# Performance work log

Measured on AMD Instinct MI355X. Metric: run time of the kernel, lower is better.

Reference implementation:

```python
import jax, jax.numpy as jnp
import numpy as np

V, E, H = 50000, 300, 512
L, N, K = 6, 8192, 4


def setup_inputs() -> dict:
    key = jax.random.key(0)
    ks = jax.random.split(key, 12)
    vocab_ix = jax.random.randint(ks[0], (L, N), 0, V)
    child_idx = jax.random.randint(ks[1], (L, N, K), 0, N)
    token_mask = jnp.ones((L, N), dtype=jnp.float32)
    child_mask = (jax.random.uniform(ks[2], (L, N, K)) < 0.75).astype(jnp.float32)
    s = 0.02
    embed = jax.random.normal(ks[3], (V, E), dtype=jnp.float32)
    W_iou = jax.random.normal(ks[4], (E, 3 * H), dtype=jnp.float32) * s
    U_iou = jax.random.normal(ks[5], (H, 3 * H), dtype=jnp.float32) * s
    b_iou = jnp.zeros((3 * H,), dtype=jnp.float32)
    W_f = jax.random.normal(ks[6], (E, H), dtype=jnp.float32) * s
    U_f = jax.random.normal(ks[7], (H, H), dtype=jnp.float32) * s
    b_f = jnp.zeros((H,), dtype=jnp.float32)
    return {"vocab_ix": vocab_ix, "child_idx": child_idx, "token_mask": token_mask,
            "child_mask": child_mask, "embed": embed, "W_iou": W_iou, "U_iou": U_iou,
            "b_iou": b_iou, "W_f": W_f, "U_f": U_f, "b_f": b_f}


def _tree_lstm(vocab_ix, child_idx, token_mask, child_mask,
               embed, W_iou, U_iou, b_iou, W_f, U_f, b_f):
    # bottom-up over levels; level L-1 = leaves (no children -> zero prev states)
    h = jnp.zeros((N, H), dtype=embed.dtype)
    c = jnp.zeros((N, H), dtype=embed.dtype)
    for l in reversed(range(L)):
        # word2vec: embedding lookup; zero vector for non-token nodes
        x = embed[vocab_ix[l]] * token_mask[l][:, None]            # [N, E]
        xWf = x @ W_f                                              # [N, H]
        if l == L - 1:
            h_tilde = jnp.zeros((N, H), dtype=x.dtype)
            fc = jnp.zeros((N, H), dtype=x.dtype)
        else:
            m = child_mask[l][:, :, None]                          # [N, K, 1]
            h_ch = h[child_idx[l]] * m                             # [N, K, H]
            c_ch = c[child_idx[l]] * m                             # [N, K, H]
            h_tilde = h_ch.sum(axis=1)                             # child-sum
            # per-child forget gates (padded slots: c_ch is 0 -> no contribution)
            f = jax.nn.sigmoid(xWf[:, None, :] + jnp.einsum('nkh,hj->nkj', h_ch, U_f) + b_f)
            fc = (f * c_ch).sum(axis=1)
        iou = x @ W_iou + h_tilde @ U_iou + b_iou                  # [N, 3H]
        i, o, u = jnp.split(iou, 3, axis=-1)
        c = jax.nn.sigmoid(i) * jnp.tanh(u) + fc
        h = jax.nn.sigmoid(o) * jnp.tanh(c)
    return h  # outputs[0][1]: hidden states of root level


def reference(vocab_ix, child_idx, token_mask, child_mask,
              embed, W_iou, U_iou, b_iou, W_f, U_f, b_f):
    return _tree_lstm(vocab_ix, child_idx, token_mask, child_mask,
                      embed, W_iou, U_iou, b_iou, W_f, U_f, b_f)
```

## Files before the change

### kernel.cpp

```cpp
#include <hip/hip_runtime.h>
#include <cmath>

#define VSZ  50000
#define EDIM 300
#define EPAD 320
#define HDIM 512
#define LVLS 6
#define NN   8192
#define KCH  4

#define BM 128
#define BN 128
#define BK 32

typedef __attribute__((ext_vector_type(8))) short bf16x8;
typedef __attribute__((ext_vector_type(8))) unsigned short us8;
typedef __attribute__((ext_vector_type(4))) float f32x4;

__device__ __forceinline__ float sigf(float x) { return 1.0f / (1.0f + expf(-x)); }

__device__ __forceinline__ unsigned short f2bf(float f) {
    unsigned u = __float_as_uint(f);
    u += 0x7FFF + ((u >> 16) & 1);
    return (unsigned short)(u >> 16);
}
__device__ __forceinline__ float bf2f(unsigned short h) {
    return __uint_as_float(((unsigned)h) << 16);
}

__device__ __forceinline__ unsigned cvt_pk_bf16(float lo, float hi) {
    unsigned r;
    asm("v_cvt_pk_bf16_f32 %0, %1, %2" : "=v"(r) : "v"(lo), "v"(hi));
    return r;
}

__global__ __launch_bounds__(256) void gconv_k(
    const float* __restrict__ embed, const int* __restrict__ vix,
    const float* __restrict__ tmask, unsigned short* __restrict__ out)
{
    int t  = blockIdx.x * 256 + threadIdx.x;
    int r  = t / (EPAD / 8);
    int j8 = (t - r * (EPAD / 8)) * 8;
    float m = tmask[r];
    int   v = vix[r];
    const float* src = embed + (size_t)v * EDIM + j8;
    us8 o;
    if (j8 + 8 <= EDIM) {
        float4 a = *(const float4*)(src);
        float4 b = *(const float4*)(src + 4);
        const float xs[8] = {a.x, a.y, a.z, a.w, b.x, b.y, b.z, b.w};
#pragma unroll
        for (int j = 0; j < 8; ++j) o[j] = f2bf(xs[j] * m);
    } else {
#pragma unroll
        for (int j = 0; j < 8; ++j) {
            float x = (j8 + j < EDIM) ? src[j] * m : 0.0f;
            o[j] = f2bf(x);
        }
    }
    *(us8*)(out + (size_t)r * EPAD + j8) = o;
}

__global__ __launch_bounds__(256) void wconv_k(
    const float* __restrict__ in, unsigned short* __restrict__ out,
    int Kreal, int Ksp, int Nd)
{
    int t = blockIdx.x * 256 + threadIdx.x;
    int k = t % Ksp;
    int n = t / Ksp;
    out[t] = (k < Kreal) ? f2bf(in[(size_t)k * Nd + n]) : (unsigned short)0;
}

#define GLL(src, dst)                                                        \
    __builtin_amdgcn_global_load_lds(                                        \
        (const __attribute__((address_space(1))) unsigned int*)(src), (dst), 16, 0, 0)

template <int EPI, int NCHUNK>
__global__ __launch_bounds__(256) void mgemm_k(
    const unsigned short* __restrict__ Ab,
    const unsigned short* __restrict__ Bt,
    const float* __restrict__ b_iou, const float* __restrict__ b_f,
    unsigned short* __restrict__ C, int ldc, int Ks)
{
    __shared__ __align__(16) unsigned short smem[6 * BM * BK];

    const int tid  = threadIdx.x;
    const int wave = tid >> 6;
    const int lane = tid & 63;
    const int quad = lane >> 4;
    const int mcol = lane & 15;
    const int wm   = (wave >> 1) * 64;
    const int wn   = (wave & 1) * 64;
    const int band = wave >> 1;

    const int GX   = gridDim.x;
    const int P    = blockIdx.x + GX * blockIdx.y;
    const int g    = P & 7;
    const int s    = P >> 3;
    const int mper = gridDim.y >> 3;
    const int sdiv = s / GX;
    const int my_mt = g * mper + sdiv;
    const int my_ng = s - sdiv * GX;
    const int tile_m = my_mt * BM;

    const int r0  = tid >> 2;
    const int kg0 = (tid & 3) ^ ((r0 >> 1) & 3);
    const int cc1 = tid + 256;
    const int r1  = cc1 >> 2;
    const int kg1 = (cc1 & 3) ^ ((r1 >> 1) & 3);

    const unsigned short* asrc0 = Ab + (size_t)(tile_m + r0) * Ks + kg0 * 8;
    const unsigned short* asrc1 = Ab + (size_t)(tile_m + r1) * Ks + kg1 * 8;

    typedef __attribute__((address_space(3))) unsigned int lds_u32;

    float* eb = reinterpret_cast<float*>(smem);
    const int erl = tid >> 3;
    const int ecg = tid & 7;

#define STAGE3(kk, bo)                                                       \
    {                                                                        \
        GLL(asrc0 + (kk), (lds_u32*)(smem + (bo) + wave * 512));             \
        GLL(asrc1 + (kk), (lds_u32*)(smem + (bo) + 2048 + wave * 512));      \
        GLL(bsrc0 + (kk), (lds_u32*)(smem + (bo) + 4096 + wave * 512));      \
        GLL(bsrc1 + (kk), (lds_u32*)(smem + (bo) + 6144 + wave * 512));      \
    }
#define WAITV4  asm volatile("s_waitcnt vmcnt(4)" ::: "memory")
#define WAITV0  asm volatile("s_waitcnt vmcnt(0)" ::: "memory")
#define BAR     __builtin_amdgcn_s_barrier()

#define COMPUTE(bo)                                                         \
    {                                                                       \
        const unsigned short* AS = smem + (bo);                             \
        const unsigned short* BS = smem + (bo) + 4096;                      \
        bf16x8 afr[4], bfr[4];                                              \
        _Pragma("unroll")                                                   \
        for (int mt = 0; mt < 4; ++mt) {                                    \
            int rw = wm + mt * 16 + mcol;                                   \
            int p  = rw * 4 + (quad ^ ((rw >> 1) & 3));                     \
            afr[mt] = *(const bf16x8*)(AS + p * 8);                         \
        }                                                                   \
        _Pragma("unroll")                                                   \
        for (int nt = 0; nt < 4; ++nt) {                                    \
            int rw = wn + nt * 16 + mcol;                                   \
            int p  = rw * 4 + (quad ^ ((rw >> 1) & 3));                     \
            bfr[nt] = *(const bf16x8*)(BS + p * 8);                         \
        }                                                                   \
        _Pragma("unroll")                                                   \
        for (int mt = 0; mt < 4; ++mt)                                      \
            _Pragma("unroll")                                               \
            for (int nt = 0; nt < 4; ++nt)                                  \
                acc[mt][nt] = __builtin_amdgcn_mfma_f32_16x16x32_bf16(      \
                    afr[mt], bfr[nt], acc[mt][nt], 0, 0, 0);                \
    }

    for (int nc = 0; nc < NCHUNK; ++nc) {
        const int tile_n = (my_ng * NCHUNK + nc) * BN;
        const unsigned short* bsrc0 = Bt + (size_t)(tile_n + r0) * Ks + kg0 * 8;
        const unsigned short* bsrc1 = Bt + (size_t)(tile_n + r1) * Ks + kg1 * 8;

        f32x4 acc[4][4] = {};
        const int nsteps = Ks / BK;

        int bo0 = 0, bo1 = 8192, bo2 = 16384;

        STAGE3(0, bo0);
        STAGE3(BK, bo1);
        WAITV4;
        BAR;

        for (int st = 0; st < nsteps; ++st) {
            const bool pf = (st + 2 < nsteps);
            if (pf) STAGE3((st + 2) * BK, bo2);
            COMPUTE(bo0);
            if (pf) { WAITV4; } else { WAITV0; }
            BAR;
            int t0 = bo0; bo0 = bo1; bo1 = bo2; bo2 = t0;
        }

#pragma unroll
        for (int mt = 0; mt < 4; ++mt) {
            const int rbase = band * 16 + quad * 4;
#pragma unroll
            for (int nt = 0; nt < 4; ++nt) {
                const int cb = wn + nt * 16 + mcol;
                const int gq = cb >> 2;
                const int cl = cb & 3;
#pragma unroll
                for (int rr = 0; rr < 4; ++rr) {
                    const int r = rbase + rr;
                    eb[r * 128 + ((gq ^ (r & 7)) << 2) + cl] = acc[mt][nt][rr];
                }
            }
            __syncthreads();

            const int grow = tile_m + (erl >> 4) * 64 + mt * 16 + (erl & 15);
            const int gcol = tile_n + ecg * 16;
            float v[16];
#pragma unroll
            for (int sxt = 0; sxt < 4; ++sxt) {
                const int pg = (ecg * 4 + sxt) ^ (erl & 7);
                f32x4 q = *(const f32x4*)&eb[erl * 128 + pg * 4];
                v[sxt * 4 + 0] = q[0]; v[sxt * 4 + 1] = q[1];
                v[sxt * 4 + 2] = q[2]; v[sxt * 4 + 3] = q[3];
            }
            if (EPI == 1) {
                const float* bp = (gcol < 3 * HDIM) ? (b_iou + gcol)
                                                    : (b_f + gcol - 3 * HDIM);
                float4 b0 = *(const float4*)(bp);
                float4 b1 = *(const float4*)(bp + 4);
                float4 b2 = *(const float4*)(bp + 8);
                float4 b3 = *(const float4*)(bp + 12);
                const float bb[16] = {b0.x, b0.y, b0.z, b0.w, b1.x, b1.y, b1.z, b1.w,
                                      b2.x, b2.y, b2.z, b2.w, b3.x, b3.y, b3.z, b3.w};
#pragma unroll
                for (int j = 0; j < 16; ++j) v[j] += bb[j];
            }
            unsigned pw[8];
#pragma unroll
            for (int j = 0; j < 8; ++j) pw[j] = cvt_pk_bf16(v[2 * j], v[2 * j + 1]);
            unsigned short* cp = C + (size_t)grow * ldc + gcol;
            *(uint4*)(cp)     = make_uint4(pw[0], pw[1], pw[2], pw[3]);
            *(uint4*)(cp + 8) = make_uint4(pw[4], pw[5], pw[6], pw[7]);
            __syncthreads();
        }
    }
#undef STAGE3
#undef WAITV4
#undef WAITV0
#undef BAR
#undef COMPUTE
}

template <bool LAST>
__global__ __launch_bounds__(256) void gatefc_k(
    const unsigned short* __restrict__ iouxW, const unsigned short* __restrict__ Z,
    const int* __restrict__ cidx, const float* __restrict__ cmask,
    const float* __restrict__ c_prev,
    float* __restrict__ c_new, unsigned short* __restrict__ hb_new,
    float* __restrict__ h_out)
{
    int t  = blockIdx.x * 256 + threadIdx.x;
    int n  = t >> 6;
    int j8 = (t & 63) << 3;
    const unsigned short* xr = iouxW + (size_t)n * 4 * HDIM + j8;
    us8 xi = *(const us8*)xr;
    us8 xo = *(const us8*)(xr + HDIM);
    us8 xu = *(const us8*)(xr + 2 * HDIM);
    us8 xf = *(const us8*)(xr + 3 * HDIM);
    float ia[8], oa[8], ua[8], xw[8], fc[8];
#pragma unroll
    for (int j = 0; j < 8; ++j) {
        ia[j] = bf2f(xi[j]); oa[j] = bf2f(xo[j]);
        ua[j] = bf2f(xu[j]); xw[j] = bf2f(xf[j]);
        fc[j] = 0.0f;
    }
    int4   ci = *(const int4*)&cidx[n * KCH];
    float4 cm = *(const float4*)&cmask[n * KCH];
    const int   cia[4] = {ci.x, ci.y, ci.z, ci.w};
    const float cma[4] = {cm.x, cm.y, cm.z, cm.w};
#pragma unroll
    for (int k = 0; k < KCH; ++k) {
        const float m = cma[k];
        const unsigned short* zr = Z + (size_t)cia[k] * 4 * HDIM + j8;
        us8 zi = *(const us8*)zr;
        us8 zo = *(const us8*)(zr + HDIM);
        us8 zu = *(const us8*)(zr + 2 * HDIM);
        us8 zf = *(const us8*)(zr + 3 * HDIM);
        const float* cpr = c_prev + (size_t)cia[k] * HDIM + j8;
        float4 ca = *(const float4*)cpr;
        float4 cb = *(const float4*)(cpr + 4);
        const float cp[8] = {ca.x, ca.y, ca.z, ca.w, cb.x, cb.y, cb.z, cb.w};
#pragma unroll
        for (int j = 0; j < 8; ++j) {
            ia[j] += m * bf2f(zi[j]);
            oa[j] += m * bf2f(zo[j]);
            ua[j] += m * bf2f(zu[j]);
            fc[j] += sigf(xw[j] + m * bf2f(zf[j])) * m * cp[j];
        }
    }
    float cv[8], hv[8];
#pragma unroll
    for (int j = 0; j < 8; ++j) {
        cv[j] = sigf(ia[j]) * tanhf(ua[j]) + fc[j];
        hv[j] = sigf(oa[j]) * tanhf(cv[j]);
    }
    if (LAST) {
        float4 h0 = make_float4(hv[0], hv[1], hv[2], hv[3]);
        float4 h1 = make_float4(hv[4], hv[5], hv[6], hv[7]);
        *(float4*)(h_out + (size_t)n * HDIM + j8)     = h0;
        *(float4*)(h_out + (size_t)n * HDIM + j8 + 4) = h1;
    } else {
        float4 c0v = make_float4(cv[0], cv[1], cv[2], cv[3]);
        float4 c1v = make_float4(cv[4], cv[5], cv[6], cv[7]);
        *(float4*)(c_new + (size_t)n * HDIM + j8)     = c0v;
        *(float4*)(c_new + (size_t)n * HDIM + j8 + 4) = c1v;
        us8 hb;
#pragma unroll
        for (int j = 0; j < 8; ++j) hb[j] = f2bf(hv[j]);
        *(us8*)(hb_new + (size_t)n * HDIM + j8) = hb;
    }
}

__global__ __launch_bounds__(256) void gateleaf_k(
    const unsigned short* __restrict__ iouxW,
    float* __restrict__ c_new, unsigned short* __restrict__ hb_new)
{
    int t  = blockIdx.x * 256 + threadIdx.x;
    int n  = t >> 6;
    int j8 = (t & 63) << 3;
    const unsigned short* xr = iouxW + (size_t)n * 4 * HDIM + j8;
    us8 xi = *(const us8*)xr;
    us8 xo = *(const us8*)(xr + HDIM);
    us8 xu = *(const us8*)(xr + 2 * HDIM);
    float cv[8], hv[8];
#pragma unroll
    for (int j = 0; j < 8; ++j) {
        cv[j] = sigf(bf2f(xi[j])) * tanhf(bf2f(xu[j]));
        hv[j] = sigf(bf2f(xo[j])) * tanhf(cv[j]);
    }
    float4 c0v = make_float4(cv[0], cv[1], cv[2], cv[3]);
    float4 c1v = make_float4(cv[4], cv[5], cv[6], cv[7]);
    *(float4*)(c_new + (size_t)n * HDIM + j8)     = c0v;
    *(float4*)(c_new + (size_t)n * HDIM + j8 + 4) = c1v;
    us8 hb;
#pragma unroll
    for (int j = 0; j < 8; ++j) hb[j] = f2bf(hv[j]);
    *(us8*)(hb_new + (size_t)n * HDIM + j8) = hb;
}

extern "C" void kernel_launch(void* const* d_in, const int* in_sizes, int n_in,
                              void* d_out, int out_size, void* d_ws, size_t ws_size,
                              hipStream_t stream)
{
    const int*   vocab_ix   = (const int*)d_in[0];
    const int*   child_idx  = (const int*)d_in[1];
    const float* token_mask = (const float*)d_in[2];
    const float* child_mask = (const float*)d_in[3];
    const float* embed      = (const float*)d_in[4];
    const float* W_iou      = (const float*)d_in[5];
    const float* U_iou      = (const float*)d_in[6];
    const float* b_iou      = (const float*)d_in[7];
    const float* W_f        = (const float*)d_in[8];
    const float* U_f        = (const float*)d_in[9];
    const float* b_f        = (const float*)d_in[10];
    float* out = (float*)d_out;

    float* ws = (float*)d_ws;
    float* c0 = ws;
    float* c1 = c0 + (size_t)NN * HDIM;
    unsigned short* usb   = (unsigned short*)(c1 + (size_t)NN * HDIM);
    unsigned short* hb0   = usb;
    unsigned short* hb1   = hb0 + (size_t)NN * HDIM;
    unsigned short* iouxW = hb1 + (size_t)NN * HDIM;
    unsigned short* Z     = iouxW + (size_t)3 * NN * 4 * HDIM;
    unsigned short* AbatA = Z + (size_t)NN * 4 * HDIM;
    unsigned short* AbatB = AbatA + (size_t)3 * NN * EPAD;
    unsigned short* WtALL = AbatB + (size_t)3 * NN * EPAD;
    unsigned short* UtALL = WtALL + (size_t)4 * HDIM * EPAD;

    dim3 blk(256);

    const int grows = 3 * NN * (EPAD / 8) / 256;
    gconv_k<<<dim3(grows), blk, 0, stream>>>(embed, vocab_ix + (size_t)3 * NN,
                                             token_mask + (size_t)3 * NN, AbatA);
    gconv_k<<<dim3(grows), blk, 0, stream>>>(embed, vocab_ix, token_mask, AbatB);
    wconv_k<<<dim3(3 * HDIM * EPAD / 256), blk, 0, stream>>>(W_iou, WtALL, EDIM, EPAD, 3 * HDIM);
    wconv_k<<<dim3(HDIM * EPAD / 256),     blk, 0, stream>>>(W_f, WtALL + (size_t)3 * HDIM * EPAD, EDIM, EPAD, HDIM);
    wconv_k<<<dim3(3 * HDIM * HDIM / 256), blk, 0, stream>>>(U_iou, UtALL, HDIM, HDIM, 3 * HDIM);
    wconv_k<<<dim3(HDIM * HDIM / 256),     blk, 0, stream>>>(U_f, UtALL + (size_t)3 * HDIM * HDIM, HDIM, HDIM, HDIM);

    unsigned short* bbuf[2] = { hb0, hb1 };
    float*          cbuf[2] = { c0,  c1  };

    const int ew_blocks = NN * HDIM / 8 / 256;

    mgemm_k<1, 2><<<dim3(8, 3 * NN / BM), blk, 0, stream>>>(
        AbatA, WtALL, b_iou, b_f, iouxW, 4 * HDIM, EPAD);

    for (int l = LVLS - 1; l >= 0; --l) {
        const int p = (LVLS - 1 - l);
        unsigned short* hb_new  = bbuf[p & 1];
        float*          c_new   = cbuf[p & 1];
        unsigned short* hb_prev = bbuf[(p & 1) ^ 1];
        float*          c_prev  = cbuf[(p & 1) ^ 1];
        const int*   cix = child_idx  + (size_t)l * NN * KCH;
        const float* cm  = child_mask + (size_t)l * NN * KCH;
        const unsigned short* ix_l =
            iouxW + (size_t)((l >= 3) ? (l - 3) : l) * NN * 4 * HDIM;

        if (l == LVLS - 1) {
            gateleaf_k<<<dim3(ew_blocks), blk, 0, stream>>>(ix_l, c_new, hb_new);
        } else {
            mgemm_k<0, 1><<<dim3(16, NN / BM), blk, 0, stream>>>(
                hb_prev, UtALL, nullptr, nullptr, Z, 4 * HDIM, HDIM);

            if (l == 0) {
                gatefc_k<true><<<dim3(ew_blocks), blk, 0, stream>>>(
                    ix_l, Z, cix, cm, c_prev, nullptr, nullptr, out);
            } else {
                gatefc_k<false><<<dim3(ew_blocks), blk, 0, stream>>>(
                    ix_l, Z, cix, cm, c_prev, c_new, hb_new, nullptr);
            }
        }

        if (l == 3) {
            mgemm_k<1, 2><<<dim3(8, 3 * NN / BM), blk, 0, stream>>>(
                AbatB, WtALL, b_iou, b_f, iouxW, 4 * HDIM, EPAD);
        }
    }
}
```

Measured before the change: 580.1 us.

## Merge prep conversion kernels and deepen GEMM LDS pipeline to four stages

The two embedding gather/convert launches become one kernel that writes both level groups (AbatA then AbatB, which sit next to each other) by remapping the row index. The four weight transpose/convert launches become a single kernel with range-based dispatch. Separately, the bf16 GEMM goes from a 3-buffer to a 4-buffer LDS ring, prefetching three K-steps ahead with matching vmcnt waits. This cuts launch overhead and hides more global-load latency, but the larger shared memory footprint can lower occupancy.

```diff
diff --git a/kernel.cpp b/kernel.cpp
--- a/kernel.cpp
+++ b/kernel.cpp
@@ -34,15 +34,16 @@
     return r;
 }
 
-__global__ __launch_bounds__(256) void gconv_k(
+__global__ __launch_bounds__(256) void gconv2_k(
     const float* __restrict__ embed, const int* __restrict__ vix,
     const float* __restrict__ tmask, unsigned short* __restrict__ out)
 {
     int t  = blockIdx.x * 256 + threadIdx.x;
     int r  = t / (EPAD / 8);
     int j8 = (t - r * (EPAD / 8)) * 8;
-    float m = tmask[r];
-    int   v = vix[r];
+    int rr = (r < 3 * NN) ? (3 * NN + r) : (r - 3 * NN);
+    float m = tmask[rr];
+    int   v = vix[rr];
     const float* src = embed + (size_t)v * EDIM + j8;
     us8 o;
     if (j8 + 8 <= EDIM) {
@@ -61,14 +62,32 @@
     *(us8*)(out + (size_t)r * EPAD + j8) = o;
 }
 
-__global__ __launch_bounds__(256) void wconv_k(
-    const float* __restrict__ in, unsigned short* __restrict__ out,
-    int Kreal, int Ksp, int Nd)
+#define WCS0 (3 * HDIM * EPAD)
+#define WCS1 (HDIM * EPAD)
+#define WCS2 (3 * HDIM * HDIM)
+#define WCS3 (HDIM * HDIM)
+__global__ __launch_bounds__(256) void wconvall_k(
+    const float* __restrict__ W_iou, const float* __restrict__ W_f,
+    const float* __restrict__ U_iou, const float* __restrict__ U_f,
+    unsigned short* __restrict__ WtALL, unsigned short* __restrict__ UtALL)
 {
     int t = blockIdx.x * 256 + threadIdx.x;
-    int k = t % Ksp;
-    int n = t / Ksp;
-    out[t] = (k < Kreal) ? f2bf(in[(size_t)k * Nd + n]) : (unsigned short)0;
+    if (t < WCS0) {
+        int k = t % EPAD, n = t / EPAD;
+        WtALL[t] = (k < EDIM) ? f2bf(W_iou[(size_t)k * (3 * HDIM) + n]) : (unsigned short)0;
+    } else if (t < WCS0 + WCS1) {
+        int u = t - WCS0;
+        int k = u % EPAD, n = u / EPAD;
+        WtALL[t] = (k < EDIM) ? f2bf(W_f[(size_t)k * HDIM + n]) : (unsigned short)0;
+    } else if (t < WCS0 + WCS1 + WCS2) {
+        int u = t - WCS0 - WCS1;
+        int k = u % HDIM, n = u / HDIM;
+        UtALL[u] = f2bf(U_iou[(size_t)k * (3 * HDIM) + n]);
+    } else {
+        int u = t - WCS0 - WCS1 - WCS2;
+        int k = u % HDIM, n = u / HDIM;
+        UtALL[WCS2 + u] = f2bf(U_f[(size_t)k * HDIM + n]);
+    }
 }
 
 #define GLL(src, dst)                                                        \
@@ -82,7 +101,7 @@
     const float* __restrict__ b_iou, const float* __restrict__ b_f,
     unsigned short* __restrict__ C, int ldc, int Ks)
 {
-    __shared__ __align__(16) unsigned short smem[6 * BM * BK];
+    __shared__ __align__(16) unsigned short smem[8 * BM * BK];
 
     const int tid  = threadIdx.x;
     const int wave = tid >> 6;
@@ -125,6 +144,7 @@
         GLL(bsrc0 + (kk), (lds_u32*)(smem + (bo) + 4096 + wave * 512));      \
         GLL(bsrc1 + (kk), (lds_u32*)(smem + (bo) + 6144 + wave * 512));      \
     }
+#define WAITV8  asm volatile("s_waitcnt vmcnt(8)" ::: "memory")
 #define WAITV4  asm volatile("s_waitcnt vmcnt(4)" ::: "memory")
 #define WAITV0  asm volatile("s_waitcnt vmcnt(0)" ::: "memory")
 #define BAR     __builtin_amdgcn_s_barrier()
@@ -162,20 +182,22 @@
         f32x4 acc[4][4] = {};
         const int nsteps = Ks / BK;
 
-        int bo0 = 0, bo1 = 8192, bo2 = 16384;
+        int bo0 = 0, bo1 = 8192, bo2 = 16384, bo3 = 24576;
 
         STAGE3(0, bo0);
         STAGE3(BK, bo1);
-        WAITV4;
+        STAGE3(2 * BK, bo2);
+        WAITV8;
         BAR;
 
         for (int st = 0; st < nsteps; ++st) {
-            const bool pf = (st + 2 < nsteps);
-            if (pf) STAGE3((st + 2) * BK, bo2);
+            if (st + 3 < nsteps) STAGE3((st + 3) * BK, bo3);
             COMPUTE(bo0);
-            if (pf) { WAITV4; } else { WAITV0; }
+            if (st + 3 < nsteps)      { WAITV8; }
+            else if (st + 2 < nsteps) { WAITV4; }
+            else                      { WAITV0; }
             BAR;
-            int t0 = bo0; bo0 = bo1; bo1 = bo2; bo2 = t0;
+            int t0 = bo0; bo0 = bo1; bo1 = bo2; bo2 = bo3; bo3 = t0;
         }
 
 #pragma unroll
@@ -226,6 +248,7 @@
         }
     }
 #undef STAGE3
+#undef WAITV8
 #undef WAITV4
 #undef WAITV0
 #undef BAR
@@ -361,14 +384,10 @@
 
     dim3 blk(256);
 
-    const int grows = 3 * NN * (EPAD / 8) / 256;
-    gconv_k<<<dim3(grows), blk, 0, stream>>>(embed, vocab_ix + (size_t)3 * NN,
-                                             token_mask + (size_t)3 * NN, AbatA);
-    gconv_k<<<dim3(grows), blk, 0, stream>>>(embed, vocab_ix, token_mask, AbatB);
-    wconv_k<<<dim3(3 * HDIM * EPAD / 256), blk, 0, stream>>>(W_iou, WtALL, EDIM, EPAD, 3 * HDIM);
-    wconv_k<<<dim3(HDIM * EPAD / 256),     blk, 0, stream>>>(W_f, WtALL + (size_t)3 * HDIM * EPAD, EDIM, EPAD, HDIM);
-    wconv_k<<<dim3(3 * HDIM * HDIM / 256), blk, 0, stream>>>(U_iou, UtALL, HDIM, HDIM, 3 * HDIM);
-    wconv_k<<<dim3(HDIM * HDIM / 256),     blk, 0, stream>>>(U_f, UtALL + (size_t)3 * HDIM * HDIM, HDIM, HDIM, HDIM);
+    gconv2_k<<<dim3(6 * NN * (EPAD / 8) / 256), blk, 0, stream>>>(
+        embed, vocab_ix, token_mask, AbatA);
+    wconvall_k<<<dim3((WCS0 + WCS1 + WCS2 + WCS3) / 256), blk, 0, stream>>>(
+        W_iou, W_f, U_iou, U_f, WtALL, UtALL);
 
     unsigned short* bbuf[2] = { hb0, hb1 };
     float*          cbuf[2] = { c0,  c1  };
```

After: 589.5 us. Within noise of the previous version (+1.6%).
